# Optimization experiments

Measured on AMD Instinct MI355X. Metric: run time of the kernel, lower is better.

## Reference

```python
import jax, jax.numpy as jnp
import numpy as np


def _cubic(x):
    absx = np.abs(x)
    absx2 = absx ** 2
    absx3 = absx ** 3
    return ((1.5 * absx3 - 2.5 * absx2 + 1) * (absx <= 1)
            + (-0.5 * absx3 + 2.5 * absx2 - 4 * absx + 2) * ((1 < absx) & (absx <= 2)))


def _contributions(in_length, out_length, scale):
    # Replicates Resizer.contributions for cubic kernel with antialiasing (scale < 1).
    kernel_width = 4.0 / scale
    fixed_kernel = lambda arg: scale * _cubic(scale * arg)
    out_coordinates = np.arange(1, out_length + 1)
    shifted = out_coordinates - (out_length - in_length * scale) / 2
    match = shifted / scale + 0.5 * (1 - 1 / scale)
    left = np.floor(match - kernel_width / 2)
    expanded = int(np.ceil(kernel_width) + 2)
    fov = np.int16(left[:, None] + np.arange(expanded) - 1)  # (out, taps)
    weights = fixed_kernel(1.0 * match[:, None] - fov - 1)
    s = np.sum(weights, axis=1)
    s[s == 0] = 1.0
    weights = weights / s[:, None]
    mirror = np.concatenate((np.arange(in_length), np.arange(in_length - 1, -1, -1)))
    fov = mirror[np.mod(fov, mirror.shape[0])]
    nz = np.nonzero(np.any(weights, axis=0))[0]  # drop all-zero taps
    return weights[:, nz], fov[:, nz]


IN_SHAPE = (32, 3, 512, 512)
OUT_HW = 256
SCALE = 0.5
NDIM_TRAIL = 3  # len(scale_factor) - 1 trailing singleton dims on weights


def setup_inputs() -> dict:
    key = jax.random.key(0)
    in_tensor = jax.random.normal(key, IN_SHAPE, dtype=jnp.float32)
    w_np, fov_np = _contributions(IN_SHAPE[2], OUT_HW, SCALE)
    taps, out_len = w_np.shape[1], w_np.shape[0]
    w = jnp.asarray(w_np.T.reshape((taps, out_len) + (1,) * NDIM_TRAIL), dtype=jnp.float32)
    fov = jnp.asarray(fov_np.T, dtype=jnp.int32)  # (taps, out)
    # H and W have identical in/out lengths and scale -> identical tables
    return {"in_tensor": in_tensor, "w2": w, "fov2": fov, "w3": w, "fov3": fov}


def reference(in_tensor, w2, fov2, w3, fov3):
    x = in_tensor
    for dim, fov, w in ((2, fov2, w2), (3, fov3, w3)):
        x = jnp.swapaxes(x, dim, 0)          # bring resized axis to front
        x = jnp.sum(x[fov] * w, axis=0)      # gather (taps,out,...) * w -> (out,...)
        x = jnp.swapaxes(x, dim, 0)
    return x
```

## Files before the change

kernel.cpp:

```cpp
#include <hip/hip_runtime.h>


#define H_IN   512
#define W_IN   512
#define H_OUT  256
#define W_OUT  256
#define BC     96
#define TAPS   8
#define OH_T   8
#define OW_T   128
#define IN_ROWS (2 * OH_T + 6)
#define MID_COLS (2 * OW_T + 6)

__device__ __forceinline__ int mir(int r, int n) {
    r = (r < 0) ? (-1 - r) : r;
    r = (r >= n) ? (2 * n - 1 - r) : r;
    return r;
}

__global__ __launch_bounds__(256) void resize_fused(const float* __restrict__ in,
                                                    const float* __restrict__ wt,
                                                    float* __restrict__ out) {
    __shared__ float mid[OH_T][MID_COLS];

    const int bid = blockIdx.x;
    const int owt = bid & 1;
    const int oht = (bid >> 1) & 31;
    const int bc  = bid >> 6;
    const int oh0 = oht * OH_T;
    const int ow0 = owt * OW_T;
    const int t   = threadIdx.x;

    float K[TAPS];
#pragma unroll
    for (int i = 0; i < TAPS; ++i) K[i] = wt[i * H_OUT];

    const float* src = in + (size_t)bc * H_IN * W_IN;
    const int rbase = 2 * oh0 - 3;
    const int cbase = 2 * ow0 - 3;

    for (int c = t; c < MID_COLS; c += 256) {
        const int gc = mir(cbase + c, W_IN);
        float acc[OH_T];
#pragma unroll
        for (int k = 0; k < OH_T; ++k) acc[k] = 0.f;

#pragma unroll
        for (int r = 0; r < IN_ROWS; ++r) {
            const float x = src[(size_t)mir(rbase + r, H_IN) * W_IN + gc];
#pragma unroll
            for (int k = 0; k < OH_T; ++k) {
                const int i = r - 2 * k;
                if (0 <= i && i < TAPS) acc[k] += K[i] * x;
            }
        }
#pragma unroll
        for (int k = 0; k < OH_T; ++k) mid[k][c] = acc[k];
    }

    __syncthreads();

    const int owl = t & (OW_T - 1);
    const int r0  = (t >> 7) * 4;
    float* dst = out + ((size_t)bc * H_OUT + oh0) * W_OUT + ow0 + owl;

#pragma unroll
    for (int rr = 0; rr < 4; ++rr) {
        const int row = r0 + rr;
        float s = 0.f;
#pragma unroll
        for (int j = 0; j < TAPS; ++j)
            s += K[j] * mid[row][2 * owl + j];
        dst[(size_t)row * W_OUT] = s;
    }
}

extern "C" void kernel_launch(void* const* d_in, const int* in_sizes, int n_in,
                              void* d_out, int out_size, void* d_ws, size_t ws_size,
                              hipStream_t stream) {
    const float* in = (const float*)d_in[0];
    const float* w2 = (const float*)d_in[1];
    float* out = (float*)d_out;
    (void)d_ws; (void)ws_size;

    resize_fused<<<BC * 32 * 2, 256, 0, stream>>>(in, w2, out);
}
```

Measured before the change: 157.4 us.

## Process full output row width per block with float2 loads and mirrored halo

Each block now covers the full 512-column input width for an 8-row output strip, with every thread loading two adjacent columns as a float2. This removes the duplicated column halo between the two horizontal tiles and the second loop pass for the extra halo columns. Mirrored edge columns are written into shared memory by the boundary threads. Output is written with nontemporal stores. The cost is half as many blocks and a larger shared tile per block.

```diff
diff --git a/kernel.cpp b/kernel.cpp
--- a/kernel.cpp
+++ b/kernel.cpp
@@ -8,9 +8,8 @@
 #define BC     96
 #define TAPS   8
 #define OH_T   8
-#define OW_T   128
 #define IN_ROWS (2 * OH_T + 6)
-#define MID_COLS (2 * OW_T + 6)
+#define MID_W  520
 
 __device__ __forceinline__ int mir(int r, int n) {
     r = (r < 0) ? (-1 - r) : r;
@@ -21,14 +20,12 @@
 __global__ __launch_bounds__(256) void resize_fused(const float* __restrict__ in,
                                                     const float* __restrict__ wt,
                                                     float* __restrict__ out) {
-    __shared__ float mid[OH_T][MID_COLS];
+    __shared__ float mid[OH_T][MID_W];
 
     const int bid = blockIdx.x;
-    const int owt = bid & 1;
-    const int oht = (bid >> 1) & 31;
-    const int bc  = bid >> 6;
+    const int oht = bid & 31;
+    const int bc  = bid >> 5;
     const int oh0 = oht * OH_T;
-    const int ow0 = owt * OW_T;
     const int t   = threadIdx.x;
 
     float K[TAPS];
@@ -37,41 +34,55 @@
 
     const float* src = in + (size_t)bc * H_IN * W_IN;
     const int rbase = 2 * oh0 - 3;
-    const int cbase = 2 * ow0 - 3;
+    const int g0 = 2 * t;
 
-    for (int c = t; c < MID_COLS; c += 256) {
-        const int gc = mir(cbase + c, W_IN);
-        float acc[OH_T];
+    float2 acc[OH_T];
 #pragma unroll
-        for (int k = 0; k < OH_T; ++k) acc[k] = 0.f;
+    for (int k = 0; k < OH_T; ++k) acc[k] = make_float2(0.f, 0.f);
 
 #pragma unroll
-        for (int r = 0; r < IN_ROWS; ++r) {
-            const float x = src[(size_t)mir(rbase + r, H_IN) * W_IN + gc];
+    for (int r = 0; r < IN_ROWS; ++r) {
+        const int gr = mir(rbase + r, H_IN);
+        const float2 x = *reinterpret_cast<const float2*>(src + (size_t)gr * W_IN + g0);
 #pragma unroll
-            for (int k = 0; k < OH_T; ++k) {
-                const int i = r - 2 * k;
-                if (0 <= i && i < TAPS) acc[k] += K[i] * x;
+        for (int k = 0; k < OH_T; ++k) {
+            const int i = r - 2 * k;
+            if (0 <= i && i < TAPS) {
+                acc[k].x += K[i] * x.x;
+                acc[k].y += K[i] * x.y;
             }
         }
+    }
+
 #pragma unroll
-        for (int k = 0; k < OH_T; ++k) mid[k][c] = acc[k];
+    for (int k = 0; k < OH_T; ++k)
+        *reinterpret_cast<float2*>(&mid[k][4 + g0]) = acc[k];
+
+    if (t == 0) {
+#pragma unroll
+        for (int k = 0; k < OH_T; ++k) { mid[k][3] = acc[k].x; mid[k][2] = acc[k].y; }
+    } else if (t == 1) {
+#pragma unroll
+        for (int k = 0; k < OH_T; ++k) mid[k][1] = acc[k].x;
+    } else if (t == 255) {
+#pragma unroll
+        for (int k = 0; k < OH_T; ++k) { mid[k][516] = acc[k].y; mid[k][517] = acc[k].x; }
+    } else if (t == 254) {
+#pragma unroll
+        for (int k = 0; k < OH_T; ++k) mid[k][518] = acc[k].y;
     }
 
     __syncthreads();
 
-    const int owl = t & (OW_T - 1);
-    const int r0  = (t >> 7) * 4;
-    float* dst = out + ((size_t)bc * H_OUT + oh0) * W_OUT + ow0 + owl;
-
+    float* dst = out + ((size_t)bc * H_OUT + oh0) * W_OUT + t;
+    const int cb = 2 * t + 1;
 #pragma unroll
-    for (int rr = 0; rr < 4; ++rr) {
-        const int row = r0 + rr;
+    for (int row = 0; row < OH_T; ++row) {
         float s = 0.f;
 #pragma unroll
         for (int j = 0; j < TAPS; ++j)
-            s += K[j] * mid[row][2 * owl + j];
-        dst[(size_t)row * W_OUT] = s;
+            s += K[j] * mid[row][cb + j];
+        __builtin_nontemporal_store(s, dst + (size_t)row * W_OUT);
     }
 }
 
@@ -83,5 +94,5 @@
     float* out = (float*)d_out;
     (void)d_ws; (void)ws_size;
 
-    resize_fused<<<BC * 32 * 2, 256, 0, stream>>>(in, w2, out);
+    resize_fused<<<BC * 32, 256, 0, stream>>>(in, w2, out);
 }
```

After: 158.7 us. About the same (+0.8%).
